# Kernel optimization log

Measured on AMD Instinct MI355X. Metric: run time of the kernel, lower is better.

## Reference

```python
import jax, jax.numpy as jnp
import numpy as np

N = 50000      # nodes
E = 800000     # edges (avg degree 16)
IN = 128       # in_features
H = 4          # num_heads
OUT = 32       # out_features per head
NEG_SLOPE = 0.2


def setup_inputs() -> dict:
    key = jax.random.key(0)
    k1, k2, k3, k4 = jax.random.split(key, 4)
    h = jax.random.normal(k1, (N, IN), dtype=jnp.float32)
    edge_index = jax.random.randint(k2, (2, E), 0, N, dtype=jnp.int32)
    # xavier-ish init scales
    W = jax.random.normal(k3, (H, IN, OUT), dtype=jnp.float32) * np.float32(np.sqrt(2.0 / (IN + OUT)))
    a = jax.random.normal(k4, (H, 2 * OUT), dtype=jnp.float32) * np.float32(np.sqrt(2.0 / (2 * OUT)))
    return {"h": h, "edge_index": edge_index, "W": W, "a": a}


def reference(h, edge_index, W, a):
    src, dst = edge_index[0], edge_index[1]
    # project per head: [N, H, OUT]
    h_proj = jnp.einsum('ni,hio->nho', h, W)
    # score = leaky_relu(a . [Wh_src || Wh_dst]) ; split a to avoid materializing the concat
    a_src, a_dst = a[:, :OUT], a[:, OUT:]
    s_src = jnp.einsum('nho,ho->nh', h_proj, a_src)   # [N, H]
    s_dst = jnp.einsum('nho,ho->nh', h_proj, a_dst)   # [N, H]
    score = jax.nn.leaky_relu(s_src[src] + s_dst[dst], negative_slope=NEG_SLOPE)  # [E, H]
    # sparse softmax over incoming edges of each dst node
    smax = jax.ops.segment_max(score, dst, num_segments=N)          # [N, H]
    smax = jnp.where(jnp.isfinite(smax), smax, jnp.float32(-1e9))   # nodes with no in-edges
    score_exp = jnp.exp(score - smax[dst])                          # [E, H]
    denom = jax.ops.segment_sum(score_exp, dst, num_segments=N)     # [N, H]
    denom = jnp.maximum(denom, jnp.float32(1e-16))
    alpha = score_exp / denom[dst]                                  # [E, H]
    # weighted aggregation (dropout is identity in eval mode)
    h_src = h_proj[src]                                             # [E, H, OUT]
    h_out = jax.ops.segment_sum(alpha[:, :, None] * h_src, dst, num_segments=N)  # [N, H, OUT]
    h_out = h_out.reshape(N, H * OUT)  # concat=True
    return jax.nn.elu(h_out)
```

## Files before the change

### kernel.cpp

```cpp
#include <hip/hip_runtime.h>

#define NEG_SLOPE 0.2f

typedef __attribute__((ext_vector_type(8))) short short8;
typedef __attribute__((ext_vector_type(4))) float floatx4;

__device__ __forceinline__ unsigned f2bf(float x) {
  unsigned u = __float_as_uint(x);
  unsigned r = ((u >> 16) & 1u) + 0x7fffu;
  return (u + r) >> 16;
}
__device__ __forceinline__ float bf2f(unsigned hi16) {
  return __uint_as_float(hi16 << 16);
}

__global__ __launch_bounds__(256) void k_gemm(const float* __restrict__ h,
                                              const float* __restrict__ W,
                                              const float* __restrict__ a,
                                              const int* __restrict__ ei,
                                              unsigned short* __restrict__ hp16,
                                              float* __restrict__ ssrc,
                                              float* __restrict__ sdst,
                                              int* __restrict__ bsize,
                                              int N, int E, int NB2) {
  __shared__ unsigned lds_u[16384];
  __shared__ int bh[256];
  const int tid = threadIdx.x;

  for (int i = tid; i < NB2; i += 256) bh[i] = 0;
  __syncthreads();
  for (long long t = (long long)blockIdx.x * 256 + tid; t < E;
       t += (long long)gridDim.x * 256)
    atomicAdd(&bh[ei[E + t] >> 8], 1);
  __syncthreads();
  for (int i = tid; i < NB2; i += 256)
    if (bh[i]) atomicAdd(&bsize[i], bh[i]);

  const int lane = tid & 63;
  const int wv = tid >> 6;
  const int quad = lane >> 4;
  const int l16 = lane & 15;

  for (int u = tid; u < 2048; u += 256) {
    int ln = u & 63;
    int kc = (u >> 6) & 3;
    int ct = u >> 8;
    int n = ct * 16 + (ln & 15);
    int kb = kc * 32 + (ln >> 4) * 8;
    int head = n >> 5;
    const float* src = W + head * 4096 + (size_t)kb * 32 + (n & 31);
    unsigned hi[4], lo[4];
#pragma unroll
    for (int jj = 0; jj < 4; ++jj) {
      float w0 = src[(2 * jj) * 32];
      float w1 = src[(2 * jj + 1) * 32];
      unsigned h0 = f2bf(w0), h1 = f2bf(w1);
      unsigned l0 = f2bf(w0 - bf2f(h0)), l1 = f2bf(w1 - bf2f(h1));
      hi[jj] = h0 | (h1 << 16);
      lo[jj] = l0 | (l1 << 16);
    }
    *(uint4*)&lds_u[u * 4] = make_uint4(hi[0], hi[1], hi[2], hi[3]);
    *(uint4*)&lds_u[8192 + u * 4] = make_uint4(lo[0], lo[1], lo[2], lo[3]);
  }

  const int row0 = blockIdx.x * 64;
  const int r = row0 + wv * 16 + l16;
  short8 Ah[4], Al[4];
#pragma unroll
  for (int kc = 0; kc < 4; ++kc) {
    float v[8];
    if (r < N) {
      float4 fa = *(const float4*)&h[(size_t)r * 128 + kc * 32 + quad * 8];
      float4 fb = *(const float4*)&h[(size_t)r * 128 + kc * 32 + quad * 8 + 4];
      v[0] = fa.x; v[1] = fa.y; v[2] = fa.z; v[3] = fa.w;
      v[4] = fb.x; v[5] = fb.y; v[6] = fb.z; v[7] = fb.w;
    } else {
#pragma unroll
      for (int j = 0; j < 8; ++j) v[j] = 0.f;
    }
#pragma unroll
    for (int j = 0; j < 8; ++j) {
      unsigned hi = f2bf(v[j]);
      Ah[kc][j] = (short)hi;
      Al[kc][j] = (short)f2bf(v[j] - bf2f(hi));
    }
  }
  __syncthreads();

  floatx4 C[8];
#pragma unroll
  for (int ct = 0; ct < 8; ++ct) {
    floatx4 c = {0.f, 0.f, 0.f, 0.f};
#pragma unroll
    for (int kc = 0; kc < 4; ++kc) {
      int bidx = ((ct * 4 + kc) * 64 + lane) * 4;
      uint4 bh4 = *(const uint4*)&lds_u[bidx];
      uint4 bl4 = *(const uint4*)&lds_u[8192 + bidx];
      short8 Bh, Bl;
      *(uint4*)&Bh = bh4;
      *(uint4*)&Bl = bl4;
      c = __builtin_amdgcn_mfma_f32_16x16x32_bf16(Ah[kc], Bh, c, 0, 0, 0);
      c = __builtin_amdgcn_mfma_f32_16x16x32_bf16(Al[kc], Bh, c, 0, 0, 0);
      c = __builtin_amdgcn_mfma_f32_16x16x32_bf16(Ah[kc], Bl, c, 0, 0, 0);
    }
    C[ct] = c;
  }
  __syncthreads();

  float* epi = (float*)lds_u;
#pragma unroll
  for (int ct = 0; ct < 8; ++ct) {
#pragma unroll
    for (int reg = 0; reg < 4; ++reg) {
      int rr = wv * 16 + quad * 4 + reg;
      epi[rr * 132 + ct * 16 + l16] = C[ct][reg];
    }
  }
  __syncthreads();

  const int row_l = tid >> 2;
  const int hh = tid & 3;
  const int rg = row0 + row_l;
  if (rg < N) {
    const float* rowp = &epi[row_l * 132 + hh * 32];
    float ss = 0.f, sd = 0.f;
    unsigned pka[16];
#pragma unroll
    for (int e = 0; e < 8; ++e) {
      float4 c4 = *(const float4*)&rowp[e * 4];
      float4 as = *(const float4*)&a[hh * 64 + e * 4];
      float4 ad = *(const float4*)&a[hh * 64 + 32 + e * 4];
      ss += c4.x * as.x + c4.y * as.y + c4.z * as.z + c4.w * as.w;
      sd += c4.x * ad.x + c4.y * ad.y + c4.z * ad.z + c4.w * ad.w;
      pka[e * 2] = f2bf(c4.x) | (f2bf(c4.y) << 16);
      pka[e * 2 + 1] = f2bf(c4.z) | (f2bf(c4.w) << 16);
    }
    unsigned short* dst = &hp16[(size_t)rg * 128 + hh * 32];
    *(uint4*)(dst) = make_uint4(pka[0], pka[1], pka[2], pka[3]);
    *(uint4*)(dst + 8) = make_uint4(pka[4], pka[5], pka[6], pka[7]);
    *(uint4*)(dst + 16) = make_uint4(pka[8], pka[9], pka[10], pka[11]);
    *(uint4*)(dst + 24) = make_uint4(pka[12], pka[13], pka[14], pka[15]);
    ssrc[(size_t)rg * 4 + hh] = ss;
    sdst[(size_t)rg * 4 + hh] = sd;
  }
}

__global__ __launch_bounds__(256) void k_scan_bk(const int* __restrict__ bsize,
                                                 int* __restrict__ bbase,
                                                 int* __restrict__ bcursor, int NB2) {
  __shared__ int lds[256];
  const int tid = threadIdx.x;
  int s = (tid < NB2) ? bsize[tid] : 0;
  lds[tid] = s;
  __syncthreads();
  for (int off = 1; off < 256; off <<= 1) {
    int t = (tid >= off) ? lds[tid - off] : 0;
    __syncthreads();
    lds[tid] += t;
    __syncthreads();
  }
  if (tid < NB2) {
    int excl = lds[tid] - s;
    bbase[tid] = excl;
    bcursor[tid] = excl;
    if (tid == NB2 - 1) bbase[NB2] = lds[tid];
  }
}

__global__ __launch_bounds__(256) void k_bin(const int* __restrict__ ei,
                                             int* __restrict__ bcursor,
                                             uint2* __restrict__ gpairs, int E, int NB2) {
  __shared__ uint2 stage[4096];
  __shared__ int cnt[256], start[256], cur[256], gbase[256];
  const int tid = threadIdx.x;
  const int e0 = blockIdx.x * 4096;
  for (int i = tid; i < NB2; i += 256) cnt[i] = 0;
  __syncthreads();
  int sarr[16], darr[16];
#pragma unroll
  for (int j = 0; j < 16; ++j) {
    int e = e0 + j * 256 + tid;
    if (e < E) {
      sarr[j] = ei[e];
      darr[j] = ei[E + e];
      atomicAdd(&cnt[darr[j] >> 8], 1);
    } else {
      darr[j] = -1;
    }
  }
  __syncthreads();
  {
    int s = (tid < NB2) ? cnt[tid] : 0;
    __shared__ int lds[256];
    lds[tid] = s;
    __syncthreads();
    for (int off = 1; off < 256; off <<= 1) {
      int t = (tid >= off) ? lds[tid - off] : 0;
      __syncthreads();
      lds[tid] += t;
      __syncthreads();
    }
    if (tid < NB2) {
      start[tid] = lds[tid] - s;
      cur[tid] = lds[tid] - s;
    }
  }
  __syncthreads();
#pragma unroll
  for (int j = 0; j < 16; ++j) {
    if (darr[j] >= 0) {
      int b = darr[j] >> 8;
      int pos = atomicAdd(&cur[b], 1);
      stage[pos] = make_uint2((unsigned)sarr[j], (unsigned)darr[j]);
    }
  }
  if (tid < NB2) {
    int c = cnt[tid];
    gbase[tid] = c ? atomicAdd(&bcursor[tid], c) : 0;
  }
  __syncthreads();
  const int total = start[NB2 - 1] + cnt[NB2 - 1];
  for (int u = tid; u < total; u += 256) {
    uint2 pr = stage[u];
    int b = (int)(pr.y >> 8);
    gpairs[gbase[b] + (u - start[b])] = pr;
  }
}

__global__ __launch_bounds__(256) void k_build(const int* __restrict__ bbase,
                                               const uint2* __restrict__ gpairs,
                                               int* __restrict__ csr_src,
                                               int* __restrict__ offs, int N) {
  __shared__ int cnt2[256], start2[256], cur2[256];
  __shared__ int srcsort[8192];
  const int tid = threadIdx.x;
  const int b = blockIdx.x;
  const int base = bbase[b];
  const int size = bbase[b + 1] - base;
  const int d0 = b << 8;
  const int ndst = min(256, N - d0);
  cnt2[tid] = 0;
  __syncthreads();
  for (int u = tid; u < size; u += 256)
    atomicAdd(&cnt2[(int)gpairs[base + u].y - d0], 1);
  __syncthreads();
  {
    int s = cnt2[tid];
    __shared__ int lds[256];
    lds[tid] = s;
    __syncthreads();
    for (int off = 1; off < 256; off <<= 1) {
      int t = (tid >= off) ? lds[tid - off] : 0;
      __syncthreads();
      lds[tid] += t;
      __syncthreads();
    }
    start2[tid] = lds[tid] - s;
    cur2[tid] = lds[tid] - s;
  }
  __syncthreads();
  for (int u = tid; u < size; u += 256) {
    uint2 pr = gpairs[base + u];
    int pos = atomicAdd(&cur2[(int)pr.y - d0], 1);
    srcsort[pos] = (int)pr.x;
  }
  __syncthreads();
  for (int u = tid; u < size; u += 256) csr_src[base + u] = srcsort[u];
  if (tid < ndst) offs[d0 + tid] = base + start2[tid] + cnt2[tid];
}

__global__ __launch_bounds__(256) void k_agg(const int* __restrict__ offs,
                                             const int* __restrict__ csr_src,
                                             const float* __restrict__ ssrc,
                                             const float* __restrict__ sdst,
                                             const uint4* __restrict__ hp4,
                                             float* __restrict__ out, int N) {
  const int t = blockIdx.x * 256 + threadIdx.x;
  const int d = t >> 4;
  if (d >= N) return;
  const int l = threadIdx.x & 15;
  const int hh = l >> 2;
  const int beg = (d == 0) ? 0 : offs[d - 1];
  const int end = offs[d];
  const float sdh = sdst[(size_t)d * 4 + hh];

  float den0 = 0.f, den1 = 0.f;
  float acc[8];
#pragma unroll
  for (int j = 0; j < 8; ++j) acc[j] = 0.f;

  int p = beg;
  for (; p + 1 < end; p += 2) {
    int s0 = csr_src[p];
    int s1 = csr_src[p + 1];
    float sc0 = ssrc[(size_t)s0 * 4 + hh] + sdh;
    float sc1 = ssrc[(size_t)s1 * 4 + hh] + sdh;
    uint4 v0 = hp4[(size_t)s0 * 16 + l];
    uint4 v1 = hp4[(size_t)s1 * 16 + l];
    sc0 = sc0 >= 0.f ? sc0 : NEG_SLOPE * sc0;
    sc1 = sc1 >= 0.f ? sc1 : NEG_SLOPE * sc1;
    float w0 = __expf(sc0);
    float w1 = __expf(sc1);
    den0 += w0;
    den1 += w1;
    acc[0] = fmaf(w0, bf2f(v0.x & 0xffffu), acc[0]);
    acc[1] = fmaf(w0, bf2f(v0.x >> 16), acc[1]);
    acc[2] = fmaf(w0, bf2f(v0.y & 0xffffu), acc[2]);
    acc[3] = fmaf(w0, bf2f(v0.y >> 16), acc[3]);
    acc[4] = fmaf(w0, bf2f(v0.z & 0xffffu), acc[4]);
    acc[5] = fmaf(w0, bf2f(v0.z >> 16), acc[5]);
    acc[6] = fmaf(w0, bf2f(v0.w & 0xffffu), acc[6]);
    acc[7] = fmaf(w0, bf2f(v0.w >> 16), acc[7]);
    acc[0] = fmaf(w1, bf2f(v1.x & 0xffffu), acc[0]);
    acc[1] = fmaf(w1, bf2f(v1.x >> 16), acc[1]);
    acc[2] = fmaf(w1, bf2f(v1.y & 0xffffu), acc[2]);
    acc[3] = fmaf(w1, bf2f(v1.y >> 16), acc[3]);
    acc[4] = fmaf(w1, bf2f(v1.z & 0xffffu), acc[4]);
    acc[5] = fmaf(w1, bf2f(v1.z >> 16), acc[5]);
    acc[6] = fmaf(w1, bf2f(v1.w & 0xffffu), acc[6]);
    acc[7] = fmaf(w1, bf2f(v1.w >> 16), acc[7]);
  }
  if (p < end) {
    int s0 = csr_src[p];
    float sc0 = ssrc[(size_t)s0 * 4 + hh] + sdh;
    uint4 v0 = hp4[(size_t)s0 * 16 + l];
    sc0 = sc0 >= 0.f ? sc0 : NEG_SLOPE * sc0;
    float w0 = __expf(sc0);
    den0 += w0;
    acc[0] = fmaf(w0, bf2f(v0.x & 0xffffu), acc[0]);
    acc[1] = fmaf(w0, bf2f(v0.x >> 16), acc[1]);
    acc[2] = fmaf(w0, bf2f(v0.y & 0xffffu), acc[2]);
    acc[3] = fmaf(w0, bf2f(v0.y >> 16), acc[3]);
    acc[4] = fmaf(w0, bf2f(v0.z & 0xffffu), acc[4]);
    acc[5] = fmaf(w0, bf2f(v0.z >> 16), acc[5]);
    acc[6] = fmaf(w0, bf2f(v0.w & 0xffffu), acc[6]);
    acc[7] = fmaf(w0, bf2f(v0.w >> 16), acc[7]);
  }
  float rden = 1.f / fmaxf(den0 + den1, 1e-16f);
  float o[8];
#pragma unroll
  for (int j = 0; j < 8; ++j) {
    float x = acc[j] * rden;
    o[j] = x > 0.f ? x : expm1f(x);
  }
  float* dst = &out[(size_t)d * 128 + l * 8];
  *(float4*)dst = make_float4(o[0], o[1], o[2], o[3]);
  *(float4*)(dst + 4) = make_float4(o[4], o[5], o[6], o[7]);
}

extern "C" void kernel_launch(void* const* d_in, const int* in_sizes, int n_in,
                              void* d_out, int out_size, void* d_ws, size_t ws_size,
                              hipStream_t stream) {
  const float* h = (const float*)d_in[0];
  const int* ei = (const int*)d_in[1];
  const float* W = (const float*)d_in[2];
  const float* a = (const float*)d_in[3];
  float* out = (float*)d_out;
  const int N = in_sizes[0] / 128;
  const int E = in_sizes[1] / 2;
  const int NB2 = (N + 255) >> 8;
  const int NB1 = (E + 4095) / 4096;

  char* ws = (char*)d_ws;
  unsigned short* hp16 = (unsigned short*)ws;
  uint2* gpairs = (uint2*)(hp16 + (size_t)N * 128);
  float* ssrc = (float*)(gpairs + (size_t)E);
  float* sdst = ssrc + (size_t)N * 4;
  int* bsize = (int*)(sdst + (size_t)N * 4);
  int* bbase = bsize + NB2;
  int* bcursor = bbase + NB2 + 1;
  int* offs = bcursor + NB2;
  int* csr_src = offs + N;

  hipMemsetAsync(bsize, 0, (size_t)NB2 * sizeof(int), stream);
  k_gemm<<<(N + 63) / 64, 256, 0, stream>>>(h, W, a, ei, hp16, ssrc, sdst, bsize, N, E, NB2);
  k_scan_bk<<<1, 256, 0, stream>>>(bsize, bbase, bcursor, NB2);
  k_bin<<<NB1, 256, 0, stream>>>(ei, bcursor, gpairs, E, NB2);
  k_build<<<NB2, 256, 0, stream>>>(bbase, gpairs, csr_src, offs, N);
  k_agg<<<(N * 16 + 255) / 256, 256, 0, stream>>>(offs, csr_src, ssrc, sdst,
                                                  (const uint4*)hp16, out, N);
}
```

Baseline: 175.5 us.

## Precompute split-bf16 weight fragments once and stage h tiles through LDS

Adds a small prep kernel that converts W into hi/lo bf16 MFMA fragments once and zeroes the bucket counters, replacing the memset. Each GEMM block then copies the precomputed fragments instead of redoing the conversion in all ~782 blocks. The h tile is loaded per k-chunk into padded LDS with coalesced float4 loads, and the MFMA loop is reordered to k-outer so A fragments are not all held in registers at once. This costs one extra kernel launch and more barriers per k-chunk, in exchange for less redundant conversion work, better-coalesced global loads and possibly fewer registers.

Result: slower. 180.0 us (+2.5%).

```diff
diff --git a/kernel.cpp b/kernel.cpp
--- a/kernel.cpp
+++ b/kernel.cpp
@@ -14,8 +14,35 @@
   return __uint_as_float(hi16 << 16);
 }
 
+__global__ __launch_bounds__(256) void k_prep(const float* __restrict__ W,
+                                              uint4* __restrict__ gWf,
+                                              int* __restrict__ bsize, int NB2) {
+  const int u = blockIdx.x * 256 + threadIdx.x;
+  if (blockIdx.x == 0 && threadIdx.x < NB2) bsize[threadIdx.x] = 0;
+  if (u >= 2048) return;
+  int ln = u & 63;
+  int kc = (u >> 6) & 3;
+  int ct = u >> 8;
+  int n = ct * 16 + (ln & 15);
+  int kb = kc * 32 + (ln >> 4) * 8;
+  int head = n >> 5;
+  const float* src = W + head * 4096 + (size_t)kb * 32 + (n & 31);
+  unsigned hi[4], lo[4];
+#pragma unroll
+  for (int jj = 0; jj < 4; ++jj) {
+    float w0 = src[(2 * jj) * 32];
+    float w1 = src[(2 * jj + 1) * 32];
+    unsigned h0 = f2bf(w0), h1 = f2bf(w1);
+    unsigned l0 = f2bf(w0 - bf2f(h0)), l1 = f2bf(w1 - bf2f(h1));
+    hi[jj] = h0 | (h1 << 16);
+    lo[jj] = l0 | (l1 << 16);
+  }
+  gWf[u] = make_uint4(hi[0], hi[1], hi[2], hi[3]);
+  gWf[2048 + u] = make_uint4(lo[0], lo[1], lo[2], lo[3]);
+}
+
 __global__ __launch_bounds__(256) void k_gemm(const float* __restrict__ h,
-                                              const float* __restrict__ W,
+                                              const uint4* __restrict__ gWf,
                                               const float* __restrict__ a,
                                               const int* __restrict__ ei,
                                               unsigned short* __restrict__ hp16,
@@ -24,6 +51,7 @@
                                               int* __restrict__ bsize,
                                               int N, int E, int NB2) {
   __shared__ unsigned lds_u[16384];
+  __shared__ float hs[64 * 36];
   __shared__ int bh[256];
   const int tid = threadIdx.x;
 
@@ -32,7 +60,11 @@
   for (long long t = (long long)blockIdx.x * 256 + tid; t < E;
        t += (long long)gridDim.x * 256)
     atomicAdd(&bh[ei[E + t] >> 8], 1);
-  __syncthreads();
+
+  for (int u = tid; u < 4096; u += 256)
+    *(uint4*)&lds_u[u * 4] = gWf[u];
+  __syncthreads();
+
   for (int i = tid; i < NB2; i += 256)
     if (bh[i]) atomicAdd(&bsize[i], bh[i]);
 
@@ -40,70 +72,45 @@
   const int wv = tid >> 6;
   const int quad = lane >> 4;
   const int l16 = lane & 15;
-
-  for (int u = tid; u < 2048; u += 256) {
-    int ln = u & 63;
-    int kc = (u >> 6) & 3;
-    int ct = u >> 8;
-    int n = ct * 16 + (ln & 15);
-    int kb = kc * 32 + (ln >> 4) * 8;
-    int head = n >> 5;
-    const float* src = W + head * 4096 + (size_t)kb * 32 + (n & 31);
-    unsigned hi[4], lo[4];
-#pragma unroll
-    for (int jj = 0; jj < 4; ++jj) {
-      float w0 = src[(2 * jj) * 32];
-      float w1 = src[(2 * jj + 1) * 32];
-      unsigned h0 = f2bf(w0), h1 = f2bf(w1);
-      unsigned l0 = f2bf(w0 - bf2f(h0)), l1 = f2bf(w1 - bf2f(h1));
-      hi[jj] = h0 | (h1 << 16);
-      lo[jj] = l0 | (l1 << 16);
-    }
-    *(uint4*)&lds_u[u * 4] = make_uint4(hi[0], hi[1], hi[2], hi[3]);
-    *(uint4*)&lds_u[8192 + u * 4] = make_uint4(lo[0], lo[1], lo[2], lo[3]);
-  }
-
   const int row0 = blockIdx.x * 64;
-  const int r = row0 + wv * 16 + l16;
-  short8 Ah[4], Al[4];
-#pragma unroll
+
+  floatx4 C[8];
+#pragma unroll
+  for (int ct = 0; ct < 8; ++ct) C[ct] = (floatx4){0.f, 0.f, 0.f, 0.f};
+
   for (int kc = 0; kc < 4; ++kc) {
-    float v[8];
-    if (r < N) {
-      float4 fa = *(const float4*)&h[(size_t)r * 128 + kc * 32 + quad * 8];
-      float4 fb = *(const float4*)&h[(size_t)r * 128 + kc * 32 + quad * 8 + 4];
-      v[0] = fa.x; v[1] = fa.y; v[2] = fa.z; v[3] = fa.w;
-      v[4] = fb.x; v[5] = fb.y; v[6] = fb.z; v[7] = fb.w;
-    } else {
-#pragma unroll
-      for (int j = 0; j < 8; ++j) v[j] = 0.f;
-    }
-#pragma unroll
-    for (int j = 0; j < 8; ++j) {
-      unsigned hi = f2bf(v[j]);
-      Ah[kc][j] = (short)hi;
-      Al[kc][j] = (short)f2bf(v[j] - bf2f(hi));
-    }
-  }
-  __syncthreads();
-
-  floatx4 C[8];
-#pragma unroll
-  for (int ct = 0; ct < 8; ++ct) {
-    floatx4 c = {0.f, 0.f, 0.f, 0.f};
-#pragma unroll
-    for (int kc = 0; kc < 4; ++kc) {
+    __syncthreads();
+    for (int idx = tid; idx < 512; idx += 256) {
+      int r = idx >> 3, c4 = idx & 7;
+      int gr = row0 + r;
+      float4 v = make_float4(0.f, 0.f, 0.f, 0.f);
+      if (gr < N) v = *(const float4*)&h[(size_t)gr * 128 + kc * 32 + c4 * 4];
+      *(float4*)&hs[r * 36 + c4 * 4] = v;
+    }
+    __syncthreads();
+    short8 Ah, Al;
+    {
+      const float* hrow = &hs[(wv * 16 + l16) * 36 + quad * 8];
+      float4 fa = *(const float4*)hrow;
+      float4 fb = *(const float4*)(hrow + 4);
+      float v[8] = {fa.x, fa.y, fa.z, fa.w, fb.x, fb.y, fb.z, fb.w};
+#pragma unroll
+      for (int j = 0; j < 8; ++j) {
+        unsigned hi = f2bf(v[j]);
+        Ah[j] = (short)hi;
+        Al[j] = (short)f2bf(v[j] - bf2f(hi));
+      }
+    }
+#pragma unroll
+    for (int ct = 0; ct < 8; ++ct) {
       int bidx = ((ct * 4 + kc) * 64 + lane) * 4;
-      uint4 bh4 = *(const uint4*)&lds_u[bidx];
-      uint4 bl4 = *(const uint4*)&lds_u[8192 + bidx];
       short8 Bh, Bl;
-      *(uint4*)&Bh = bh4;
-      *(uint4*)&Bl = bl4;
-      c = __builtin_amdgcn_mfma_f32_16x16x32_bf16(Ah[kc], Bh, c, 0, 0, 0);
-      c = __builtin_amdgcn_mfma_f32_16x16x32_bf16(Al[kc], Bh, c, 0, 0, 0);
-      c = __builtin_amdgcn_mfma_f32_16x16x32_bf16(Ah[kc], Bl, c, 0, 0, 0);
-    }
-    C[ct] = c;
+      *(uint4*)&Bh = *(const uint4*)&lds_u[bidx];
+      *(uint4*)&Bl = *(const uint4*)&lds_u[8192 + bidx];
+      C[ct] = __builtin_amdgcn_mfma_f32_16x16x32_bf16(Ah, Bh, C[ct], 0, 0, 0);
+      C[ct] = __builtin_amdgcn_mfma_f32_16x16x32_bf16(Al, Bh, C[ct], 0, 0, 0);
+      C[ct] = __builtin_amdgcn_mfma_f32_16x16x32_bf16(Ah, Bl, C[ct], 0, 0, 0);
+    }
   }
   __syncthreads();
 
@@ -362,7 +369,8 @@
   const int NB1 = (E + 4095) / 4096;
 
   char* ws = (char*)d_ws;
-  unsigned short* hp16 = (unsigned short*)ws;
+  uint4* gWf = (uint4*)ws;
+  unsigned short* hp16 = (unsigned short*)(gWf + 4096);
   uint2* gpairs = (uint2*)(hp16 + (size_t)N * 128);
   float* ssrc = (float*)(gpairs + (size_t)E);
   float* sdst = ssrc + (size_t)N * 4;
@@ -372,8 +380,8 @@
   int* offs = bcursor + NB2;
   int* csr_src = offs + N;
 
-  hipMemsetAsync(bsize, 0, (size_t)NB2 * sizeof(int), stream);
-  k_gemm<<<(N + 63) / 64, 256, 0, stream>>>(h, W, a, ei, hp16, ssrc, sdst, bsize, N, E, NB2);
+  k_prep<<<8, 256, 0, stream>>>(W, gWf, bsize, NB2);
+  k_gemm<<<(N + 63) / 64, 256, 0, stream>>>(h, gWf, a, ei, hp16, ssrc, sdst, bsize, N, E, NB2);
   k_scan_bk<<<1, 256, 0, stream>>>(bsize, bbase, bcursor, NB2);
   k_bin<<<NB1, 256, 0, stream>>>(ei, bcursor, gpairs, E, NB2);
   k_build<<<NB2, 256, 0, stream>>>(bbase, gpairs, csr_src, offs, N);
```

## Precompute split-bf16 W once and use per-block count table for deterministic binning

Applied to the files above, without the earlier changes.

Moves the W hi/lo bf16 conversion out of every GEMM block into a small prep kernel whose packed result is copied into LDS. It also replaces the histogram fused into the GEMM (plus global atomics and a memset) with a separate count kernel, a single-block scan producing per-block bin offsets, and atomic-free placement in k_bin. This removes redundant per-block W conversion and the edge histogram from the GEMM's critical path. In exchange it adds two extra launches and a serial loop over about 196 blocks in a single-block scan.

Measured after the change: 234.4 us. 1.34x slower.

```diff
diff --git a/kernel.cpp b/kernel.cpp
--- a/kernel.cpp
+++ b/kernel.cpp
@@ -14,54 +14,46 @@
   return __uint_as_float(hi16 << 16);
 }
 
+__global__ __launch_bounds__(256) void k_prep(const float* __restrict__ W,
+                                              uint4* __restrict__ gWf) {
+  const int u = blockIdx.x * 256 + threadIdx.x;
+  if (u >= 2048) return;
+  int ln = u & 63;
+  int kc = (u >> 6) & 3;
+  int ct = u >> 8;
+  int n = ct * 16 + (ln & 15);
+  int kb = kc * 32 + (ln >> 4) * 8;
+  int head = n >> 5;
+  const float* src = W + head * 4096 + (size_t)kb * 32 + (n & 31);
+  unsigned hi[4], lo[4];
+#pragma unroll
+  for (int jj = 0; jj < 4; ++jj) {
+    float w0 = src[(2 * jj) * 32];
+    float w1 = src[(2 * jj + 1) * 32];
+    unsigned h0 = f2bf(w0), h1 = f2bf(w1);
+    unsigned l0 = f2bf(w0 - bf2f(h0)), l1 = f2bf(w1 - bf2f(h1));
+    hi[jj] = h0 | (h1 << 16);
+    lo[jj] = l0 | (l1 << 16);
+  }
+  gWf[u] = make_uint4(hi[0], hi[1], hi[2], hi[3]);
+  gWf[2048 + u] = make_uint4(lo[0], lo[1], lo[2], lo[3]);
+}
+
 __global__ __launch_bounds__(256) void k_gemm(const float* __restrict__ h,
-                                              const float* __restrict__ W,
+                                              const uint4* __restrict__ gWf,
                                               const float* __restrict__ a,
-                                              const int* __restrict__ ei,
                                               unsigned short* __restrict__ hp16,
                                               float* __restrict__ ssrc,
-                                              float* __restrict__ sdst,
-                                              int* __restrict__ bsize,
-                                              int N, int E, int NB2) {
+                                              float* __restrict__ sdst, int N) {
   __shared__ unsigned lds_u[16384];
-  __shared__ int bh[256];
-  const int tid = threadIdx.x;
-
-  for (int i = tid; i < NB2; i += 256) bh[i] = 0;
-  __syncthreads();
-  for (long long t = (long long)blockIdx.x * 256 + tid; t < E;
-       t += (long long)gridDim.x * 256)
-    atomicAdd(&bh[ei[E + t] >> 8], 1);
-  __syncthreads();
-  for (int i = tid; i < NB2; i += 256)
-    if (bh[i]) atomicAdd(&bsize[i], bh[i]);
-
+  const int tid = threadIdx.x;
   const int lane = tid & 63;
   const int wv = tid >> 6;
   const int quad = lane >> 4;
   const int l16 = lane & 15;
 
-  for (int u = tid; u < 2048; u += 256) {
-    int ln = u & 63;
-    int kc = (u >> 6) & 3;
-    int ct = u >> 8;
-    int n = ct * 16 + (ln & 15);
-    int kb = kc * 32 + (ln >> 4) * 8;
-    int head = n >> 5;
-    const float* src = W + head * 4096 + (size_t)kb * 32 + (n & 31);
-    unsigned hi[4], lo[4];
-#pragma unroll
-    for (int jj = 0; jj < 4; ++jj) {
-      float w0 = src[(2 * jj) * 32];
-      float w1 = src[(2 * jj + 1) * 32];
-      unsigned h0 = f2bf(w0), h1 = f2bf(w1);
-      unsigned l0 = f2bf(w0 - bf2f(h0)), l1 = f2bf(w1 - bf2f(h1));
-      hi[jj] = h0 | (h1 << 16);
-      lo[jj] = l0 | (l1 << 16);
-    }
-    *(uint4*)&lds_u[u * 4] = make_uint4(hi[0], hi[1], hi[2], hi[3]);
-    *(uint4*)&lds_u[8192 + u * 4] = make_uint4(lo[0], lo[1], lo[2], lo[3]);
-  }
+  for (int u = tid; u < 4096; u += 256)
+    *(uint4*)&lds_u[u * 4] = gWf[u];
 
   const int row0 = blockIdx.x * 64;
   const int r = row0 + wv * 16 + l16;
@@ -94,11 +86,9 @@
 #pragma unroll
     for (int kc = 0; kc < 4; ++kc) {
       int bidx = ((ct * 4 + kc) * 64 + lane) * 4;
-      uint4 bh4 = *(const uint4*)&lds_u[bidx];
-      uint4 bl4 = *(const uint4*)&lds_u[8192 + bidx];
       short8 Bh, Bl;
-      *(uint4*)&Bh = bh4;
-      *(uint4*)&Bl = bl4;
+      *(uint4*)&Bh = *(const uint4*)&lds_u[bidx];
+      *(uint4*)&Bl = *(const uint4*)&lds_u[8192 + bidx];
       c = __builtin_amdgcn_mfma_f32_16x16x32_bf16(Ah[kc], Bh, c, 0, 0, 0);
       c = __builtin_amdgcn_mfma_f32_16x16x32_bf16(Al[kc], Bh, c, 0, 0, 0);
       c = __builtin_amdgcn_mfma_f32_16x16x32_bf16(Ah[kc], Bl, c, 0, 0, 0);
@@ -145,13 +135,36 @@
   }
 }
 
-__global__ __launch_bounds__(256) void k_scan_bk(const int* __restrict__ bsize,
+__global__ __launch_bounds__(256) void k_count(const int* __restrict__ ei,
+                                               int* __restrict__ gcnt, int E, int NB2) {
+  __shared__ int cnt[256];
+  const int tid = threadIdx.x;
+  const int e0 = blockIdx.x * 4096;
+  for (int i = tid; i < NB2; i += 256) cnt[i] = 0;
+  __syncthreads();
+#pragma unroll
+  for (int j = 0; j < 16; ++j) {
+    int e = e0 + j * 256 + tid;
+    if (e < E) atomicAdd(&cnt[ei[E + e] >> 8], 1);
+  }
+  __syncthreads();
+  for (int i = tid; i < NB2; i += 256) gcnt[blockIdx.x * NB2 + i] = cnt[i];
+}
+
+__global__ __launch_bounds__(256) void k_scanall(int* __restrict__ gcnt,
                                                  int* __restrict__ bbase,
-                                                 int* __restrict__ bcursor, int NB2) {
+                                                 int NB1, int NB2, int E) {
   __shared__ int lds[256];
   const int tid = threadIdx.x;
-  int s = (tid < NB2) ? bsize[tid] : 0;
-  lds[tid] = s;
+  int run = 0;
+  if (tid < NB2) {
+    for (int blk = 0; blk < NB1; ++blk) {
+      int c = gcnt[blk * NB2 + tid];
+      gcnt[blk * NB2 + tid] = run;
+      run += c;
+    }
+  }
+  lds[tid] = (tid < NB2) ? run : 0;
   __syncthreads();
   for (int off = 1; off < 256; off <<= 1) {
     int t = (tid >= off) ? lds[tid - off] : 0;
@@ -160,15 +173,15 @@
     __syncthreads();
   }
   if (tid < NB2) {
-    int excl = lds[tid] - s;
+    int excl = lds[tid] - run;
     bbase[tid] = excl;
-    bcursor[tid] = excl;
-    if (tid == NB2 - 1) bbase[NB2] = lds[tid];
+    if (tid == NB2 - 1) bbase[NB2] = E;
+    for (int blk = 0; blk < NB1; ++blk) gcnt[blk * NB2 + tid] += excl;
   }
 }
 
 __global__ __launch_bounds__(256) void k_bin(const int* __restrict__ ei,
-                                             int* __restrict__ bcursor,
+                                             const int* __restrict__ gcnt,
                                              uint2* __restrict__ gpairs, int E, int NB2) {
   __shared__ uint2 stage[4096];
   __shared__ int cnt[256], start[256], cur[256], gbase[256];
@@ -203,6 +216,7 @@
     if (tid < NB2) {
       start[tid] = lds[tid] - s;
       cur[tid] = lds[tid] - s;
+      gbase[tid] = gcnt[blockIdx.x * NB2 + tid];
     }
   }
   __syncthreads();
@@ -213,10 +227,6 @@
       int pos = atomicAdd(&cur[b], 1);
       stage[pos] = make_uint2((unsigned)sarr[j], (unsigned)darr[j]);
     }
-  }
-  if (tid < NB2) {
-    int c = cnt[tid];
-    gbase[tid] = c ? atomicAdd(&bcursor[tid], c) : 0;
   }
   __syncthreads();
   const int total = start[NB2 - 1] + cnt[NB2 - 1];
@@ -362,20 +372,21 @@
   const int NB1 = (E + 4095) / 4096;
 
   char* ws = (char*)d_ws;
-  unsigned short* hp16 = (unsigned short*)ws;
+  uint4* gWf = (uint4*)ws;
+  unsigned short* hp16 = (unsigned short*)(gWf + 4096);
   uint2* gpairs = (uint2*)(hp16 + (size_t)N * 128);
   float* ssrc = (float*)(gpairs + (size_t)E);
   float* sdst = ssrc + (size_t)N * 4;
-  int* bsize = (int*)(sdst + (size_t)N * 4);
-  int* bbase = bsize + NB2;
-  int* bcursor = bbase + NB2 + 1;
-  int* offs = bcursor + NB2;
+  int* gcnt = (int*)(sdst + (size_t)N * 4);
+  int* bbase = gcnt + (size_t)NB1 * NB2;
+  int* offs = bbase + NB2 + 1;
   int* csr_src = offs + N;
 
-  hipMemsetAsync(bsize, 0, (size_t)NB2 * sizeof(int), stream);
-  k_gemm<<<(N + 63) / 64, 256, 0, stream>>>(h, W, a, ei, hp16, ssrc, sdst, bsize, N, E, NB2);
-  k_scan_bk<<<1, 256, 0, stream>>>(bsize, bbase, bcursor, NB2);
-  k_bin<<<NB1, 256, 0, stream>>>(ei, bcursor, gpairs, E, NB2);
+  k_prep<<<8, 256, 0, stream>>>(W, gWf);
+  k_gemm<<<(N + 63) / 64, 256, 0, stream>>>(h, gWf, a, hp16, ssrc, sdst, N);
+  k_count<<<NB1, 256, 0, stream>>>(ei, gcnt, E, NB2);
+  k_scanall<<<1, 256, 0, stream>>>(gcnt, bbase, NB1, NB2, E);
+  k_bin<<<NB1, 256, 0, stream>>>(ei, gcnt, gpairs, E, NB2);
   k_build<<<NB2, 256, 0, stream>>>(bbase, gpairs, csr_src, offs, N);
   k_agg<<<(N * 16 + 255) / 256, 256, 0, stream>>>(offs, csr_src, ssrc, sdst,
                                                   (const uint4*)hp16, out, N);
```
